# Performance work log

Hardware: AMD Instinct MI355X
Metric: run time of the kernel (lower is better)

The kernel has to match this reference:

```python
import jax, jax.numpy as jnp
import numpy as np

B, N, D, E, H = 2, 1024, 768, 128, 16
HD = D // H
INF = 1.0e6


def setup_inputs() -> dict:
    key = jax.random.key(0)
    ks = jax.random.split(key, 12)
    s = 0.02
    return {
        "node_embed": jax.random.normal(ks[0], (B, N, D), jnp.float32),
        "edge_embed": jax.random.normal(ks[1], (B, N, N, E), jnp.float32),
        "node_mask": jnp.ones((B, N), jnp.int32),
        "k_in": jax.random.normal(ks[2], (B, N, D), jnp.float32),
        "Wq": jax.random.normal(ks[3], (D, D), jnp.float32) * s,
        "bq": jnp.zeros((D,), jnp.float32),
        "Wk": jax.random.normal(ks[4], (D, D), jnp.float32) * s,
        "Wv": jax.random.normal(ks[5], (D, D), jnp.float32) * s,
        "Wg": jax.random.normal(ks[6], (D, D), jnp.float32) * s,
        "ln_g": jnp.ones((E,), jnp.float32),
        "ln_b": jnp.zeros((E,), jnp.float32),
        "Wz": jax.random.normal(ks[7], (E, H), jnp.float32) * s,
        "Wo": jax.random.normal(ks[8], (D, D), jnp.float32) * s,
    }


def reference(node_embed, edge_embed, node_mask, k_in,
              Wq, bq, Wk, Wv, Wg, ln_g, ln_b, Wz, Wo):
    b, n, d = node_embed.shape
    h = Wz.shape[1]
    hd = d // h
    # projections (torch Linear: x @ W.T + b)
    q = (node_embed @ Wq.T + bq).reshape(b, n, h, hd)
    k = (k_in @ Wk.T).reshape(b, n, h, hd)
    v = (k_in @ Wv.T).reshape(b, n, h, hd)
    g = jax.nn.sigmoid(node_embed @ Wg.T)  # (b,n,d)
    # pair bias: LayerNorm over edge_dim -> Linear(E->H) -> (b,h,i,j)
    mu = edge_embed.mean(-1, keepdims=True)
    var = edge_embed.var(-1, keepdims=True)
    zn = (edge_embed - mu) * jax.lax.rsqrt(var + 1e-5) * ln_g + ln_b
    bias = jnp.einsum('bije,eh->bhij', zn, Wz)
    # attention in fp32
    attn = jnp.einsum('bihd,bjhd->bhij', q, k) / np.sqrt(hd).astype(np.float32)
    attn = attn + bias
    attn = attn + (1.0 - node_mask[:, None, None, :].astype(jnp.float32)) * (-INF)
    attn = jax.nn.softmax(attn, axis=-1)
    o = jnp.einsum('bhij,bjhd->bihd', attn, v).reshape(b, n, d)
    return (g * o) @ Wo.T
```

## Files before the change

### kernel.cpp

```cpp
#include <hip/hip_runtime.h>
#include <hip/hip_bf16.h>

#define B_ 2
#define N_ 1024
#define D_ 768
#define E_ 128
#define H_ 16
#define HD_ 48
#define HDP_ 64

typedef short bf16x8 __attribute__((ext_vector_type(8)));
typedef float f32x4 __attribute__((ext_vector_type(4)));

__device__ __forceinline__ unsigned short f2bf(float f) {
    __hip_bfloat16 h = __float2bfloat16(f);
    return *reinterpret_cast<unsigned short*>(&h);
}
__device__ __forceinline__ float bf2f(unsigned short s) {
    return __uint_as_float(((unsigned int)s) << 16);
}

__device__ __forceinline__ void stage_tile(const float* __restrict__ edge,
                                           size_t row0, float* etbuf,
                                           int w, int lane)
{
#pragma unroll
    for (int u = 0; u < 8; ++u) {
        const int row = w * 16 + u * 2 + (lane >> 5);
        const int sl = (lane & 31) ^ (row & 7);
        const float* src = edge + (row0 + row) * E_ + (sl << 2);
        float* dst = etbuf + (w * 16 + u * 2) * E_;
        __builtin_amdgcn_global_load_lds(
            (const __attribute__((address_space(1))) void*)src,
            (__attribute__((address_space(3))) void*)dst, 16, 0, 0);
    }
}

__device__ __forceinline__ void stage64(const unsigned short* __restrict__ src,
                                        int row0, int k0,
                                        unsigned short* tile, int w, int lane)
{
#pragma unroll
    for (int u = 0; u < 2; ++u) {
        const int rloc = (lane >> 3);
        const int row = w * 16 + u * 8 + rloc;
        const int ch = (lane & 7) ^ rloc;
        const unsigned short* s = src + (size_t)(row0 + row) * D_ + k0 + ch * 8;
        unsigned short* d = tile + (w * 16 + u * 8) * 64;
        __builtin_amdgcn_global_load_lds(
            (const __attribute__((address_space(1))) void*)s,
            (__attribute__((address_space(3))) void*)d, 16, 0, 0);
    }
}

#define LDF(tile, r, gc) \
    (*(const bf16x8*)&(tile)[(size_t)(r) * 64 + ((((gc) ^ ((r) & 7))) << 3)])

__global__ __launch_bounds__(256, 2) void bias_conv_kernel(
    const float* __restrict__ edge, const float* __restrict__ lng,
    const float* __restrict__ lnb, const float* __restrict__ Wz,
    const int* __restrict__ mask, unsigned short* __restrict__ bias,
    const float* __restrict__ node, const float* __restrict__ kin,
    const float* __restrict__ Wq, const float* __restrict__ Wk,
    const float* __restrict__ Wv, const float* __restrict__ Wg,
    const float* __restrict__ Wo,
    unsigned short* __restrict__ nb, unsigned short* __restrict__ kb,
    unsigned short* __restrict__ WqB, unsigned short* __restrict__ WkB,
    unsigned short* __restrict__ WvB, unsigned short* __restrict__ WgB,
    unsigned short* __restrict__ Whi, unsigned short* __restrict__ Wlo,
    unsigned short* __restrict__ qp, unsigned short* __restrict__ kp)
{
    const int tid = threadIdx.x;
    const int lane = tid & 63;
    const int w = tid >> 6;
    const int lr = lane & 15, lg = lane >> 4;

    __shared__ __align__(16) float et[2][64 * E_];

    if (blockIdx.x >= 2048) {
        const int c = blockIdx.x - 2048;
        for (int u = c * 256 + tid; u < 1589248; u += 131072) {
            if (u < 786432) {
                const int y01 = u / 393216;
                const int idx4 = (u - y01 * 393216) * 4;
                const float* s = y01 ? kin : node;
                unsigned short* d = y01 ? kb : nb;
                const float4 v = *(const float4*)(s + idx4);
                ushort4 o;
                o.x = f2bf(v.x); o.y = f2bf(v.y); o.z = f2bf(v.z); o.w = f2bf(v.w);
                *(ushort4*)(d + idx4) = o;
            } else if (u < 1523712) {
                const int u2 = u - 786432;
                const int w5 = u2 / 147456;
                const int idx4 = (u2 - w5 * 147456) * 4;
                if (w5 < 4) {
                    const float* s = (w5 == 0) ? Wq : (w5 == 1) ? Wk :
                                     (w5 == 2) ? Wv : Wg;
                    unsigned short* d = (w5 == 0) ? WqB : (w5 == 1) ? WkB :
                                        (w5 == 2) ? WvB : WgB;
                    const float4 v = *(const float4*)(s + idx4);
                    ushort4 o;
                    o.x = f2bf(v.x); o.y = f2bf(v.y);
                    o.z = f2bf(v.z); o.w = f2bf(v.w);
                    *(ushort4*)(d + idx4) = o;
                } else {
                    const float4 v = *(const float4*)(Wo + idx4);
                    ushort4 hi, lo;
                    hi.x = f2bf(v.x); lo.x = f2bf(v.x - bf2f(hi.x));
                    hi.y = f2bf(v.y); lo.y = f2bf(v.y - bf2f(hi.y));
                    hi.z = f2bf(v.z); lo.z = f2bf(v.z - bf2f(hi.z));
                    hi.w = f2bf(v.w); lo.w = f2bf(v.w - bf2f(hi.w));
                    *(ushort4*)(Whi + idx4) = hi;
                    *(ushort4*)(Wlo + idx4) = lo;
                }
            } else {
                const int u3 = u - 1523712;
                const int row = u3 >> 1, half = u3 & 1;
                uint4 z = {0u, 0u, 0u, 0u};
                *(uint4*)(qp + ((size_t)row << 6) + 48 + half * 8) = z;
                *(uint4*)(kp + ((size_t)row << 6) + 48 + half * 8) = z;
            }
        }
        return;
    }

    bf16x8 wzf[4];
#pragma unroll
    for (int ks = 0; ks < 4; ++ks)
#pragma unroll
        for (int e = 0; e < 8; ++e)
            wzf[ks][e] = (short)f2bf(Wz[(ks * 32 + lg * 8 + e) * H_ + lr]);

    size_t t = blockIdx.x;
    stage_tile(edge, t * 64, et[0], w, lane);
    __syncthreads();

    for (int it = 0; it < 16; ++it) {
        float* cbuf = et[it & 1];
        float* nbuf = et[(it & 1) ^ 1];
        if (it < 15) stage_tile(edge, (t + 2048) * 64, nbuf, w, lane);

        const int row = w * 16 + lr;
        const int rx = row & 7;
        const float* xr = cbuf + row * E_;
        float x[4][8];
        float s = 0.f, sq = 0.f;
#pragma unroll
        for (int ks = 0; ks < 4; ++ks) {
            const int s0 = ks * 8 + lg * 2;
            const float4 a = *(const float4*)(xr + ((s0 ^ rx) << 2));
            const float4 bb = *(const float4*)(xr + (((s0 + 1) ^ rx) << 2));
            x[ks][0] = a.x; x[ks][1] = a.y; x[ks][2] = a.z; x[ks][3] = a.w;
            x[ks][4] = bb.x; x[ks][5] = bb.y; x[ks][6] = bb.z; x[ks][7] = bb.w;
#pragma unroll
            for (int e = 0; e < 8; ++e) { s += x[ks][e]; sq = fmaf(x[ks][e], x[ks][e], sq); }
        }
        s  += __shfl_xor(s, 16);  s  += __shfl_xor(s, 32);
        sq += __shfl_xor(sq, 16); sq += __shfl_xor(sq, 32);
        const float mean = s * (1.f / 128.f);
        const float var = sq * (1.f / 128.f) - mean * mean;
        const float rs = rsqrtf(var + 1e-5f);
        const float c0 = -mean * rs;

        f32x4 acc = {};
#pragma unroll
        for (int ks = 0; ks < 4; ++ks) {
            bf16x8 af;
#pragma unroll
            for (int e = 0; e < 8; ++e) {
                const int ee = ks * 32 + lg * 8 + e;
                const float zn = fmaf(fmaf(x[ks][e], rs, c0), lng[ee], lnb[ee]);
                af[e] = (short)f2bf(zn);
            }
            acc = __builtin_amdgcn_mfma_f32_16x16x32_bf16(af, wzf[ks], acc, 0, 0, 0);
        }

        const int b = (int)(t >> 14);
        const int i = (int)((t >> 4) & 1023);
        const int j = (int)((t & 15) << 6) + w * 16 + lg * 4;
        const int4 mv = *(const int4*)(mask + b * N_ + j);
        const int* mvp = (const int*)&mv;
        ushort4 pk;
        pk.x = f2bf(acc[0] + (1.f - (float)mvp[0]) * (-1.0e6f));
        pk.y = f2bf(acc[1] + (1.f - (float)mvp[1]) * (-1.0e6f));
        pk.z = f2bf(acc[2] + (1.f - (float)mvp[2]) * (-1.0e6f));
        pk.w = f2bf(acc[3] + (1.f - (float)mvp[3]) * (-1.0e6f));
        *(ushort4*)(bias + (((size_t)((b * H_ + lr) * N_ + i)) << 10) + j) = pk;

        __syncthreads();
        t += 2048;
    }
}

__global__ __launch_bounds__(256) void proj2_kernel(
    const unsigned short* __restrict__ nb, const unsigned short* __restrict__ kb,
    const unsigned short* __restrict__ WqB, const unsigned short* __restrict__ WkB,
    const unsigned short* __restrict__ WvB, const unsigned short* __restrict__ WgB,
    const float* __restrict__ bq,
    unsigned short* __restrict__ qp, unsigned short* __restrict__ kp,
    unsigned short* __restrict__ vT, float* __restrict__ g)
{
    const int pair = blockIdx.z;
    const int tid = threadIdx.x;
    const int lane = tid & 63;
    const int w = tid >> 6;
    const int wm = w >> 1, wn = w & 1;
    const int lr = lane & 15, lg = lane >> 4;
    const int mbase = blockIdx.x * 64;
    const int nbase = blockIdx.y * 64;

    const unsigned short* A  = pair ? kb  : nb;
    const unsigned short* W1 = pair ? WkB : WqB;
    const unsigned short* W2 = pair ? WvB : WgB;

    __shared__ __align__(16) unsigned short st[2][3][64 * 64];

    f32x4 acc1[2][2] = {};
    f32x4 acc2[2][2] = {};

    stage64(A,  mbase, 0, st[0][0], w, lane);
    stage64(W1, nbase, 0, st[0][1], w, lane);
    stage64(W2, nbase, 0, st[0][2], w, lane);
    __syncthreads();

    for (int ks = 0; ks < 12; ++ks) {
        unsigned short (*cb)[4096] = st[ks & 1];
        if (ks < 11) {
            unsigned short (*nbuf)[4096] = st[(ks & 1) ^ 1];
            const int k1 = (ks + 1) * 64;
            stage64(A,  mbase, k1, nbuf[0], w, lane);
            stage64(W1, nbase, k1, nbuf[1], w, lane);
            stage64(W2, nbase, k1, nbuf[2], w, lane);
        }
#pragma unroll
        for (int hf = 0; hf < 2; ++hf) {
            bf16x8 af[2], w1f[2], w2f[2];
#pragma unroll
            for (int ms = 0; ms < 2; ++ms)
                af[ms] = LDF(cb[0], wm * 32 + ms * 16 + lr, hf * 4 + lg);
#pragma unroll
            for (int ns = 0; ns < 2; ++ns) {
                w1f[ns] = LDF(cb[1], wn * 32 + ns * 16 + lr, hf * 4 + lg);
                w2f[ns] = LDF(cb[2], wn * 32 + ns * 16 + lr, hf * 4 + lg);
            }
#pragma unroll
            for (int ms = 0; ms < 2; ++ms)
#pragma unroll
                for (int ns = 0; ns < 2; ++ns) {
                    acc1[ms][ns] = __builtin_amdgcn_mfma_f32_16x16x32_bf16(
                        af[ms], w1f[ns], acc1[ms][ns], 0, 0, 0);
                    if (pair == 0)
                        acc2[ms][ns] = __builtin_amdgcn_mfma_f32_16x16x32_bf16(
                            af[ms], w2f[ns], acc2[ms][ns], 0, 0, 0);
                    else
                        acc2[ns][ms] = __builtin_amdgcn_mfma_f32_16x16x32_bf16(
                            w2f[ns], af[ms], acc2[ns][ms], 0, 0, 0);
                }
        }
        __syncthreads();
    }

    unsigned short* t1 = &st[0][0][0];
    unsigned short* t2 = &st[0][1][0];
    float* gt = (float*)&st[0][1][0];

    float bqv[2] = {0.f, 0.f};
    if (pair == 0) {
#pragma unroll
        for (int ns = 0; ns < 2; ++ns)
            bqv[ns] = bq[nbase + wn * 32 + ns * 16 + lr];
    }

#pragma unroll
    for (int ms = 0; ms < 2; ++ms)
#pragma unroll
        for (int ns = 0; ns < 2; ++ns)
#pragma unroll
            for (int r = 0; r < 4; ++r) {
                const int row = wm * 32 + ms * 16 + lg * 4 + r;
                const int col = wn * 32 + ns * 16 + lr;
                t1[row * 64 + col] = f2bf(acc1[ms][ns][r] + bqv[ns]);
                if (pair == 0)
                    gt[row * 64 + col] = 1.f / (1.f + __expf(-acc2[ms][ns][r]));
                else {
                    const int drow = wn * 32 + ns * 16 + lg * 4 + r;
                    const int tcol = wm * 32 + ms * 16 + lr;
                    t2[drow * 64 + tcol] = f2bf(acc2[ns][ms][r]);
                }
            }
    __syncthreads();

    const int b = mbase >> 10;
    const int tok0 = mbase & 1023;
    unsigned short* dst1 = (pair == 0) ? qp : kp;
    for (int c = tid; c < 512; c += 256) {
        const int row = c >> 3, ch = (c & 7) * 8;
        const int colg = nbase + ch;
        const int h = colg / HD_, hd = colg - h * HD_;
        *(uint4*)(dst1 + (((size_t)((b * H_ + h) * N_ + tok0 + row)) << 6) + hd) =
            *(const uint4*)&t1[row * 64 + ch];
    }
    if (pair == 0) {
        for (int c = tid; c < 1024; c += 256) {
            const int row = c >> 4, ch = (c & 15) * 4;
            *(float4*)(g + (size_t)(mbase + row) * D_ + nbase + ch) =
                *(const float4*)&gt[row * 64 + ch];
        }
    } else {
        for (int c = tid; c < 512; c += 256) {
            const int dl = c >> 3, tch = (c & 7) * 8;
            const int dg = nbase + dl;
            const int h = dg / HD_, hd = dg - h * HD_;
            *(uint4*)(vT + (((size_t)((b * H_ + h) * HD_ + hd)) << 10) + tok0 + tch) =
                *(const uint4*)&t2[dl * 64 + tch];
        }
    }
}

__global__ __launch_bounds__(256) void attn_kernel(
    const unsigned short* __restrict__ qp, const unsigned short* __restrict__ kp,
    const unsigned short* __restrict__ vT, const unsigned short* __restrict__ bias,
    const float* __restrict__ g,
    unsigned short* __restrict__ Xhi, unsigned short* __restrict__ Xlo)
{
    const int tid = threadIdx.x;
    const int w = tid >> 6;
    const int lane = tid & 63;
    const int lr = lane & 15, lg = lane >> 4;
    const int bh = blockIdx.x >> 6;
    const int it = blockIdx.x & 63;
    const int b = bh >> 4;
    const int h = bh & 15;
    const int i0 = it * 16;
    const float scale = 0.14433756729740643f;

    __shared__ unsigned short pt[4][16][40];
    __shared__ float comb[3][64][13];

    bf16x8 qf0, qf1;
    {
        const unsigned short* qb = qp + (((size_t)bh * N_ + i0 + lr) << 6) + lg * 8;
        qf0 = *(const bf16x8*)qb;
        qf1 = *(const bf16x8*)(qb + 32);
    }

    float li = 0.f;
    f32x4 ov[3] = {};
    const unsigned short* biasrow =
        bias + ((size_t)bh << 20) + ((size_t)(i0 + lr) << 10);

    const int jlo = w * 256;
    for (int j0 = jlo; j0 < jlo + 256; j0 += 32) {
#pragma unroll
        for (int s = 0; s < 2; ++s) {
            const unsigned short* kb =
                kp + (((size_t)bh * N_ + j0 + s * 16 + lr) << 6) + lg * 8;
            bf16x8 k0 = *(const bf16x8*)kb;
            bf16x8 k1 = *(const bf16x8*)(kb + 32);
            f32x4 tacc = {};
            tacc = __builtin_amdgcn_mfma_f32_16x16x32_bf16(k0, qf0, tacc, 0, 0, 0);
            tacc = __builtin_amdgcn_mfma_f32_16x16x32_bf16(k1, qf1, tacc, 0, 0, 0);
            const ushort4 bv = *(const ushort4*)(biasrow + j0 + s * 16 + lg * 4);
            const unsigned short* bvp = (const unsigned short*)&bv;
            float p[4];
#pragma unroll
            for (int r = 0; r < 4; ++r) {
                p[r] = __expf(fmaf(tacc[r], scale, bf2f(bvp[r])));
                li += p[r];
            }
            ushort4 pk;
            pk.x = f2bf(p[0]); pk.y = f2bf(p[1]);
            pk.z = f2bf(p[2]); pk.w = f2bf(p[3]);
            *(ushort4*)&pt[w][lr][s * 16 + lg * 4] = pk;
        }
        bf16x8 pa = *(const bf16x8*)&pt[w][lr][lg * 8];
#pragma unroll
        for (int v = 0; v < 3; ++v) {
            const unsigned short* vb =
                vT + (((size_t)(bh * HD_ + v * 16 + lr)) << 10) + j0 + lg * 8;
            bf16x8 vf = *(const bf16x8*)vb;
            ov[v] = __builtin_amdgcn_mfma_f32_16x16x32_bf16(pa, vf, ov[v], 0, 0, 0);
        }
    }

    if (w > 0) {
        float* cb = &comb[w - 1][lane][0];
#pragma unroll
        for (int v = 0; v < 3; ++v)
#pragma unroll
            for (int r = 0; r < 4; ++r) cb[v * 4 + r] = ov[v][r];
        cb[12] = li;
    }
    __syncthreads();
    if (w == 0) {
#pragma unroll
        for (int s = 0; s < 3; ++s) {
            const float* cb = &comb[s][lane][0];
#pragma unroll
            for (int v = 0; v < 3; ++v)
#pragma unroll
                for (int r = 0; r < 4; ++r) ov[v][r] += cb[v * 4 + r];
            li += cb[12];
        }
        li += __shfl_xor(li, 16);
        li += __shfl_xor(li, 32);
        float lired[4];
#pragma unroll
        for (int r = 0; r < 4; ++r) lired[r] = __shfl(li, lg * 4 + r);

#pragma unroll
        for (int v = 0; v < 3; ++v) {
#pragma unroll
            for (int r = 0; r < 4; ++r) {
                const size_t row = (size_t)(b * N_ + i0 + lg * 4 + r);
                const int col = h * HD_ + v * 16 + lr;
                const float xv = g[row * D_ + col] * (ov[v][r] / lired[r]);
                const unsigned short hi = f2bf(xv);
                const size_t off = row * D_ + col;
                Xhi[off] = hi;
                Xlo[off] = f2bf(xv - bf2f(hi));
            }
        }
    }
}

__global__ __launch_bounds__(256) void out_gemm(
    const unsigned short* __restrict__ Xhi, const unsigned short* __restrict__ Xlo,
    const unsigned short* __restrict__ Whi, const unsigned short* __restrict__ Wlo,
    float* __restrict__ out)
{
    const int tid = threadIdx.x;
    const int lane = tid & 63;
    const int w = tid >> 6;
    const int wm = w >> 1, wn = w & 1;
    const int lr = lane & 15, lg = lane >> 4;
    const int mbase = blockIdx.x * 64;
    const int nbase = blockIdx.y * 64;

    __shared__ __align__(16) unsigned short st[2][4][64 * 64];

    f32x4 acc[2][2] = {};

    stage64(Xhi, mbase, 0, st[0][0], w, lane);
    stage64(Xlo, mbase, 0, st[0][1], w, lane);
    stage64(Whi, nbase, 0, st[0][2], w, lane);
    stage64(Wlo, nbase, 0, st[0][3], w, lane);
    __syncthreads();

    for (int ks = 0; ks < 12; ++ks) {
        unsigned short (*cb)[4096] = st[ks & 1];
        if (ks < 11) {
            unsigned short (*nbuf)[4096] = st[(ks & 1) ^ 1];
            const int k1 = (ks + 1) * 64;
            stage64(Xhi, mbase, k1, nbuf[0], w, lane);
            stage64(Xlo, mbase, k1, nbuf[1], w, lane);
            stage64(Whi, nbase, k1, nbuf[2], w, lane);
            stage64(Wlo, nbase, k1, nbuf[3], w, lane);
        }
#pragma unroll
        for (int hf = 0; hf < 2; ++hf) {
            bf16x8 ah[2], al[2], bh[2], bl[2];
#pragma unroll
            for (int ms = 0; ms < 2; ++ms) {
                ah[ms] = LDF(cb[0], wm * 32 + ms * 16 + lr, hf * 4 + lg);
                al[ms] = LDF(cb[1], wm * 32 + ms * 16 + lr, hf * 4 + lg);
            }
#pragma unroll
            for (int ns = 0; ns < 2; ++ns) {
                bh[ns] = LDF(cb[2], wn * 32 + ns * 16 + lr, hf * 4 + lg);
                bl[ns] = LDF(cb[3], wn * 32 + ns * 16 + lr, hf * 4 + lg);
            }
#pragma unroll
            for (int ms = 0; ms < 2; ++ms)
#pragma unroll
                for (int ns = 0; ns < 2; ++ns) {
                    acc[ms][ns] = __builtin_amdgcn_mfma_f32_16x16x32_bf16(ah[ms], bh[ns], acc[ms][ns], 0, 0, 0);
                    acc[ms][ns] = __builtin_amdgcn_mfma_f32_16x16x32_bf16(ah[ms], bl[ns], acc[ms][ns], 0, 0, 0);
                    acc[ms][ns] = __builtin_amdgcn_mfma_f32_16x16x32_bf16(al[ms], bh[ns], acc[ms][ns], 0, 0, 0);
                }
        }
        __syncthreads();
    }

#pragma unroll
    for (int ms = 0; ms < 2; ++ms)
#pragma unroll
        for (int ns = 0; ns < 2; ++ns)
#pragma unroll
            for (int r = 0; r < 4; ++r)
                out[(size_t)(mbase + wm * 32 + ms * 16 + lg * 4 + r) * D_ +
                    nbase + wn * 32 + ns * 16 + lr] = acc[ms][ns][r];
}

extern "C" void kernel_launch(void* const* d_in, const int* in_sizes, int n_in,
                              void* d_out, int out_size, void* d_ws, size_t ws_size,
                              hipStream_t stream) {
    const float* node = (const float*)d_in[0];
    const float* edge = (const float*)d_in[1];
    const int*   mask = (const int*)d_in[2];
    const float* kin  = (const float*)d_in[3];
    const float* Wq   = (const float*)d_in[4];
    const float* bq   = (const float*)d_in[5];
    const float* Wk   = (const float*)d_in[6];
    const float* Wv   = (const float*)d_in[7];
    const float* Wg   = (const float*)d_in[8];
    const float* lng  = (const float*)d_in[9];
    const float* lnb  = (const float*)d_in[10];
    const float* Wz   = (const float*)d_in[11];
    const float* Wo   = (const float*)d_in[12];
    float* out = (float*)d_out;

    char* ws = (char*)d_ws;
    const size_t qk_bytes = (size_t)B_ * H_ * N_ * HDP_ * 2;
    unsigned short* qp = (unsigned short*)ws;   ws += qk_bytes;
    unsigned short* kp = (unsigned short*)ws;   ws += qk_bytes;
    unsigned short* vT = (unsigned short*)ws;   ws += (size_t)B_ * H_ * HD_ * N_ * 2;
    float* gbuf = (float*)ws;                   ws += (size_t)B_ * N_ * D_ * 4;
    unsigned short* bias = (unsigned short*)ws; ws += (size_t)B_ * H_ * N_ * N_ * 2;
    unsigned short* Xhi = (unsigned short*)ws;  ws += (size_t)B_ * N_ * D_ * 2;
    unsigned short* Xlo = (unsigned short*)ws;  ws += (size_t)B_ * N_ * D_ * 2;
    unsigned short* Whi = (unsigned short*)ws;  ws += (size_t)D_ * D_ * 2;
    unsigned short* Wlo = (unsigned short*)ws;  ws += (size_t)D_ * D_ * 2;
    unsigned short* nb  = (unsigned short*)ws;  ws += (size_t)B_ * N_ * D_ * 2;
    unsigned short* kb  = (unsigned short*)ws;  ws += (size_t)B_ * N_ * D_ * 2;
    unsigned short* WqB = (unsigned short*)ws;  ws += (size_t)D_ * D_ * 2;
    unsigned short* WkB = (unsigned short*)ws;  ws += (size_t)D_ * D_ * 2;
    unsigned short* WvB = (unsigned short*)ws;  ws += (size_t)D_ * D_ * 2;
    unsigned short* WgB = (unsigned short*)ws;  ws += (size_t)D_ * D_ * 2;

    bias_conv_kernel<<<dim3(2560), 256, 0, stream>>>(
        edge, lng, lnb, Wz, mask, bias,
        node, kin, Wq, Wk, Wv, Wg, Wo,
        nb, kb, WqB, WkB, WvB, WgB, Whi, Wlo, qp, kp);
    proj2_kernel<<<dim3(32, 12, 2), 256, 0, stream>>>(
        nb, kb, WqB, WkB, WvB, WgB, bq, qp, kp, vT, gbuf);
    attn_kernel<<<dim3(2048), 256, 0, stream>>>(qp, kp, vT, bias, gbuf, Xhi, Xlo);
    out_gemm<<<dim3(32, 12), 256, 0, stream>>>(Xhi, Xlo, Whi, Wlo, out);
}
```

Baseline: 329.0 us.

## Fuse QKVG projection into bias kernel with on-the-fly bf16 conversion

Merges the projection GEMM into the edge-bias kernel as extra blocks. Those blocks load fp32 node/k_in and weights directly, convert them to bf16 in registers, and stage them in shared memory. This drops the separate conversion pass, its bf16 intermediate buffers and one kernel launch, and lets the projection run alongside the bandwidth-bound bias work. In the attention kernel, the bias row loads are also hoisted ahead of the loop and the P tile is double-buffered. The costs are higher register pressure and 64KB of shared memory per block, which may reduce occupancy.

```diff
diff --git a/kernel.cpp b/kernel.cpp
--- a/kernel.cpp
+++ b/kernel.cpp
@@ -56,65 +56,187 @@
 #define LDF(tile, r, gc) \
     (*(const bf16x8*)&(tile)[(size_t)(r) * 64 + ((((gc) ^ ((r) & 7))) << 3)])
 
-__global__ __launch_bounds__(256, 2) void bias_conv_kernel(
+__global__ __launch_bounds__(256, 2) void fused_kernel(
     const float* __restrict__ edge, const float* __restrict__ lng,
     const float* __restrict__ lnb, const float* __restrict__ Wz,
     const int* __restrict__ mask, unsigned short* __restrict__ bias,
     const float* __restrict__ node, const float* __restrict__ kin,
     const float* __restrict__ Wq, const float* __restrict__ Wk,
     const float* __restrict__ Wv, const float* __restrict__ Wg,
-    const float* __restrict__ Wo,
-    unsigned short* __restrict__ nb, unsigned short* __restrict__ kb,
-    unsigned short* __restrict__ WqB, unsigned short* __restrict__ WkB,
-    unsigned short* __restrict__ WvB, unsigned short* __restrict__ WgB,
+    const float* __restrict__ Wo, const float* __restrict__ bq,
     unsigned short* __restrict__ Whi, unsigned short* __restrict__ Wlo,
-    unsigned short* __restrict__ qp, unsigned short* __restrict__ kp)
+    unsigned short* __restrict__ qp, unsigned short* __restrict__ kp,
+    unsigned short* __restrict__ vT, float* __restrict__ g)
 {
     const int tid = threadIdx.x;
     const int lane = tid & 63;
     const int w = tid >> 6;
     const int lr = lane & 15, lg = lane >> 4;
 
-    __shared__ __align__(16) float et[2][64 * E_];
-
-    if (blockIdx.x >= 2048) {
-        const int c = blockIdx.x - 2048;
-        for (int u = c * 256 + tid; u < 1589248; u += 131072) {
-            if (u < 786432) {
-                const int y01 = u / 393216;
-                const int idx4 = (u - y01 * 393216) * 4;
-                const float* s = y01 ? kin : node;
-                unsigned short* d = y01 ? kb : nb;
-                const float4 v = *(const float4*)(s + idx4);
-                ushort4 o;
-                o.x = f2bf(v.x); o.y = f2bf(v.y); o.z = f2bf(v.z); o.w = f2bf(v.w);
-                *(ushort4*)(d + idx4) = o;
-            } else if (u < 1523712) {
-                const int u2 = u - 786432;
-                const int w5 = u2 / 147456;
-                const int idx4 = (u2 - w5 * 147456) * 4;
-                if (w5 < 4) {
-                    const float* s = (w5 == 0) ? Wq : (w5 == 1) ? Wk :
-                                     (w5 == 2) ? Wv : Wg;
-                    unsigned short* d = (w5 == 0) ? WqB : (w5 == 1) ? WkB :
-                                        (w5 == 2) ? WvB : WgB;
-                    const float4 v = *(const float4*)(s + idx4);
-                    ushort4 o;
-                    o.x = f2bf(v.x); o.y = f2bf(v.y);
-                    o.z = f2bf(v.z); o.w = f2bf(v.w);
-                    *(ushort4*)(d + idx4) = o;
-                } else {
-                    const float4 v = *(const float4*)(Wo + idx4);
-                    ushort4 hi, lo;
-                    hi.x = f2bf(v.x); lo.x = f2bf(v.x - bf2f(hi.x));
-                    hi.y = f2bf(v.y); lo.y = f2bf(v.y - bf2f(hi.y));
-                    hi.z = f2bf(v.z); lo.z = f2bf(v.z - bf2f(hi.z));
-                    hi.w = f2bf(v.w); lo.w = f2bf(v.w - bf2f(hi.w));
-                    *(ushort4*)(Whi + idx4) = hi;
-                    *(ushort4*)(Wlo + idx4) = lo;
+    __shared__ __align__(16) unsigned char smem[65536];
+
+    if (blockIdx.x < 768) {
+        const int pair = blockIdx.x / 384;
+        const int rem = blockIdx.x - pair * 384;
+        const int mbase = (rem & 31) * 64;
+        const int nbase = (rem >> 5) * 64;
+        const int wm = w >> 1, wn = w & 1;
+
+        const float* A  = pair ? kin : node;
+        const float* W1 = pair ? Wk : Wq;
+        const float* W2 = pair ? Wv : Wg;
+        unsigned short* sbase = (unsigned short*)smem;
+
+        float4 ld[3][2][2];
+        auto issue = [&](int k0) {
+#pragma unroll
+            for (int t = 0; t < 3; ++t) {
+                const float* src = (t == 0) ? A : (t == 1) ? W1 : W2;
+                const int rb = (t == 0) ? mbase : nbase;
+#pragma unroll
+                for (int u = 0; u < 2; ++u) {
+                    const int uu = tid * 2 + u;
+                    const int row = uu >> 3, ch = uu & 7;
+                    const float* s = src + (size_t)(rb + row) * D_ + k0 + ch * 8;
+                    ld[t][u][0] = *(const float4*)s;
+                    ld[t][u][1] = *(const float4*)(s + 4);
                 }
+            }
+        };
+        auto commit = [&](unsigned short* base) {
+#pragma unroll
+            for (int t = 0; t < 3; ++t) {
+#pragma unroll
+                for (int u = 0; u < 2; ++u) {
+                    const int uu = tid * 2 + u;
+                    const int row = uu >> 3, ch = uu & 7;
+                    bf16x8 v;
+                    v[0] = (short)f2bf(ld[t][u][0].x);
+                    v[1] = (short)f2bf(ld[t][u][0].y);
+                    v[2] = (short)f2bf(ld[t][u][0].z);
+                    v[3] = (short)f2bf(ld[t][u][0].w);
+                    v[4] = (short)f2bf(ld[t][u][1].x);
+                    v[5] = (short)f2bf(ld[t][u][1].y);
+                    v[6] = (short)f2bf(ld[t][u][1].z);
+                    v[7] = (short)f2bf(ld[t][u][1].w);
+                    *(bf16x8*)&base[t * 4096 + row * 64 + ((ch ^ (row & 7)) << 3)] = v;
+                }
+            }
+        };
+
+        f32x4 acc1[2][2] = {};
+        f32x4 acc2[2][2] = {};
+
+        issue(0);
+        commit(sbase);
+        __syncthreads();
+
+        for (int ks = 0; ks < 12; ++ks) {
+            unsigned short* cb = sbase + (ks & 1) * 12288;
+            unsigned short* nb2 = sbase + ((ks & 1) ^ 1) * 12288;
+            if (ks < 11) issue((ks + 1) * 64);
+#pragma unroll
+            for (int hf = 0; hf < 2; ++hf) {
+                bf16x8 af[2], w1f[2], w2f[2];
+#pragma unroll
+                for (int ms = 0; ms < 2; ++ms)
+                    af[ms] = LDF(cb, wm * 32 + ms * 16 + lr, hf * 4 + lg);
+#pragma unroll
+                for (int ns = 0; ns < 2; ++ns) {
+                    w1f[ns] = LDF(cb + 4096, wn * 32 + ns * 16 + lr, hf * 4 + lg);
+                    w2f[ns] = LDF(cb + 8192, wn * 32 + ns * 16 + lr, hf * 4 + lg);
+                }
+#pragma unroll
+                for (int ms = 0; ms < 2; ++ms)
+#pragma unroll
+                    for (int ns = 0; ns < 2; ++ns) {
+                        acc1[ms][ns] = __builtin_amdgcn_mfma_f32_16x16x32_bf16(
+                            af[ms], w1f[ns], acc1[ms][ns], 0, 0, 0);
+                        if (pair == 0)
+                            acc2[ms][ns] = __builtin_amdgcn_mfma_f32_16x16x32_bf16(
+                                af[ms], w2f[ns], acc2[ms][ns], 0, 0, 0);
+                        else
+                            acc2[ns][ms] = __builtin_amdgcn_mfma_f32_16x16x32_bf16(
+                                w2f[ns], af[ms], acc2[ns][ms], 0, 0, 0);
+                    }
+            }
+            if (ks < 11) commit(nb2);
+            __syncthreads();
+        }
+
+        unsigned short* t1 = sbase;
+        unsigned short* t2 = sbase + 4096;
+        float* gt = (float*)(sbase + 4096);
+
+        float bqv[2] = {0.f, 0.f};
+        if (pair == 0) {
+#pragma unroll
+            for (int ns = 0; ns < 2; ++ns)
+                bqv[ns] = bq[nbase + wn * 32 + ns * 16 + lr];
+        }
+
+#pragma unroll
+        for (int ms = 0; ms < 2; ++ms)
+#pragma unroll
+            for (int ns = 0; ns < 2; ++ns)
+#pragma unroll
+                for (int r = 0; r < 4; ++r) {
+                    const int row = wm * 32 + ms * 16 + lg * 4 + r;
+                    const int col = wn * 32 + ns * 16 + lr;
+                    t1[row * 64 + col] = f2bf(acc1[ms][ns][r] + bqv[ns]);
+                    if (pair == 0)
+                        gt[row * 64 + col] = 1.f / (1.f + __expf(-acc2[ms][ns][r]));
+                    else {
+                        const int drow = wn * 32 + ns * 16 + lg * 4 + r;
+                        const int tcol = wm * 32 + ms * 16 + lr;
+                        t2[drow * 64 + tcol] = f2bf(acc2[ns][ms][r]);
+                    }
+                }
+        __syncthreads();
+
+        const int b = mbase >> 10;
+        const int tok0 = mbase & 1023;
+        unsigned short* dst1 = (pair == 0) ? qp : kp;
+        for (int c = tid; c < 512; c += 256) {
+            const int row = c >> 3, ch = (c & 7) * 8;
+            const int colg = nbase + ch;
+            const int h = colg / HD_, hd = colg - h * HD_;
+            *(uint4*)(dst1 + (((size_t)((b * H_ + h) * N_ + tok0 + row)) << 6) + hd) =
+                *(const uint4*)&t1[row * 64 + ch];
+        }
+        if (pair == 0) {
+            for (int c = tid; c < 1024; c += 256) {
+                const int row = c >> 4, ch = (c & 15) * 4;
+                *(float4*)(g + (size_t)(mbase + row) * D_ + nbase + ch) =
+                    *(const float4*)&gt[row * 64 + ch];
+            }
+        } else {
+            for (int c = tid; c < 512; c += 256) {
+                const int dl = c >> 3, tch = (c & 7) * 8;
+                const int dg = nbase + dl;
+                const int h = dg / HD_, hd = dg - h * HD_;
+                *(uint4*)(vT + (((size_t)((b * H_ + h) * HD_ + hd)) << 10) + tok0 + tch) =
+                    *(const uint4*)&t2[dl * 64 + tch];
+            }
+        }
+        return;
+    }
+
+    if (blockIdx.x >= 2816) {
+        const int c = blockIdx.x - 2816;
+        for (int u = c * 256 + tid; u < 212992; u += 32768) {
+            if (u < 147456) {
+                const int i4 = u * 4;
+                const float4 v = *(const float4*)(Wo + i4);
+                ushort4 hi, lo;
+                hi.x = f2bf(v.x); lo.x = f2bf(v.x - bf2f(hi.x));
+                hi.y = f2bf(v.y); lo.y = f2bf(v.y - bf2f(hi.y));
+                hi.z = f2bf(v.z); lo.z = f2bf(v.z - bf2f(hi.z));
+                hi.w = f2bf(v.w); lo.w = f2bf(v.w - bf2f(hi.w));
+                *(ushort4*)(Whi + i4) = hi;
+                *(ushort4*)(Wlo + i4) = lo;
             } else {
-                const int u3 = u - 1523712;
+                const int u3 = u - 147456;
                 const int row = u3 >> 1, half = u3 & 1;
                 uint4 z = {0u, 0u, 0u, 0u};
                 *(uint4*)(qp + ((size_t)row << 6) + 48 + half * 8) = z;
@@ -124,6 +246,9 @@
         return;
     }
 
+    float* e0 = (float*)smem;
+    float* e1 = e0 + 64 * E_;
+
     bf16x8 wzf[4];
 #pragma unroll
     for (int ks = 0; ks < 4; ++ks)
@@ -131,13 +256,13 @@
         for (int e = 0; e < 8; ++e)
             wzf[ks][e] = (short)f2bf(Wz[(ks * 32 + lg * 8 + e) * H_ + lr]);
 
-    size_t t = blockIdx.x;
-    stage_tile(edge, t * 64, et[0], w, lane);
+    size_t t = blockIdx.x - 768;
+    stage_tile(edge, t * 64, e0, w, lane);
     __syncthreads();
 
     for (int it = 0; it < 16; ++it) {
-        float* cbuf = et[it & 1];
-        float* nbuf = et[(it & 1) ^ 1];
+        float* cbuf = (it & 1) ? e1 : e0;
+        float* nbuf = (it & 1) ? e0 : e1;
         if (it < 15) stage_tile(edge, (t + 2048) * 64, nbuf, w, lane);
 
         const int row = w * 16 + lr;
@@ -189,131 +314,6 @@
 
         __syncthreads();
         t += 2048;
-    }
-}
-
-__global__ __launch_bounds__(256) void proj2_kernel(
-    const unsigned short* __restrict__ nb, const unsigned short* __restrict__ kb,
-    const unsigned short* __restrict__ WqB, const unsigned short* __restrict__ WkB,
-    const unsigned short* __restrict__ WvB, const unsigned short* __restrict__ WgB,
-    const float* __restrict__ bq,
-    unsigned short* __restrict__ qp, unsigned short* __restrict__ kp,
-    unsigned short* __restrict__ vT, float* __restrict__ g)
-{
-    const int pair = blockIdx.z;
-    const int tid = threadIdx.x;
-    const int lane = tid & 63;
-    const int w = tid >> 6;
-    const int wm = w >> 1, wn = w & 1;
-    const int lr = lane & 15, lg = lane >> 4;
-    const int mbase = blockIdx.x * 64;
-    const int nbase = blockIdx.y * 64;
-
-    const unsigned short* A  = pair ? kb  : nb;
-    const unsigned short* W1 = pair ? WkB : WqB;
-    const unsigned short* W2 = pair ? WvB : WgB;
-
-    __shared__ __align__(16) unsigned short st[2][3][64 * 64];
-
-    f32x4 acc1[2][2] = {};
-    f32x4 acc2[2][2] = {};
-
-    stage64(A,  mbase, 0, st[0][0], w, lane);
-    stage64(W1, nbase, 0, st[0][1], w, lane);
-    stage64(W2, nbase, 0, st[0][2], w, lane);
-    __syncthreads();
-
-    for (int ks = 0; ks < 12; ++ks) {
-        unsigned short (*cb)[4096] = st[ks & 1];
-        if (ks < 11) {
-            unsigned short (*nbuf)[4096] = st[(ks & 1) ^ 1];
-            const int k1 = (ks + 1) * 64;
-            stage64(A,  mbase, k1, nbuf[0], w, lane);
-            stage64(W1, nbase, k1, nbuf[1], w, lane);
-            stage64(W2, nbase, k1, nbuf[2], w, lane);
-        }
-#pragma unroll
-        for (int hf = 0; hf < 2; ++hf) {
-            bf16x8 af[2], w1f[2], w2f[2];
-#pragma unroll
-            for (int ms = 0; ms < 2; ++ms)
-                af[ms] = LDF(cb[0], wm * 32 + ms * 16 + lr, hf * 4 + lg);
-#pragma unroll
-            for (int ns = 0; ns < 2; ++ns) {
-                w1f[ns] = LDF(cb[1], wn * 32 + ns * 16 + lr, hf * 4 + lg);
-                w2f[ns] = LDF(cb[2], wn * 32 + ns * 16 + lr, hf * 4 + lg);
-            }
-#pragma unroll
-            for (int ms = 0; ms < 2; ++ms)
-#pragma unroll
-                for (int ns = 0; ns < 2; ++ns) {
-                    acc1[ms][ns] = __builtin_amdgcn_mfma_f32_16x16x32_bf16(
-                        af[ms], w1f[ns], acc1[ms][ns], 0, 0, 0);
-                    if (pair == 0)
-                        acc2[ms][ns] = __builtin_amdgcn_mfma_f32_16x16x32_bf16(
-                            af[ms], w2f[ns], acc2[ms][ns], 0, 0, 0);
-                    else
-                        acc2[ns][ms] = __builtin_amdgcn_mfma_f32_16x16x32_bf16(
-                            w2f[ns], af[ms], acc2[ns][ms], 0, 0, 0);
-                }
-        }
-        __syncthreads();
-    }
-
-    unsigned short* t1 = &st[0][0][0];
-    unsigned short* t2 = &st[0][1][0];
-    float* gt = (float*)&st[0][1][0];
-
-    float bqv[2] = {0.f, 0.f};
-    if (pair == 0) {
-#pragma unroll
-        for (int ns = 0; ns < 2; ++ns)
-            bqv[ns] = bq[nbase + wn * 32 + ns * 16 + lr];
-    }
-
-#pragma unroll
-    for (int ms = 0; ms < 2; ++ms)
-#pragma unroll
-        for (int ns = 0; ns < 2; ++ns)
-#pragma unroll
-            for (int r = 0; r < 4; ++r) {
-                const int row = wm * 32 + ms * 16 + lg * 4 + r;
-                const int col = wn * 32 + ns * 16 + lr;
-                t1[row * 64 + col] = f2bf(acc1[ms][ns][r] + bqv[ns]);
-                if (pair == 0)
-                    gt[row * 64 + col] = 1.f / (1.f + __expf(-acc2[ms][ns][r]));
-                else {
-                    const int drow = wn * 32 + ns * 16 + lg * 4 + r;
-                    const int tcol = wm * 32 + ms * 16 + lr;
-                    t2[drow * 64 + tcol] = f2bf(acc2[ns][ms][r]);
-                }
-            }
-    __syncthreads();
-
-    const int b = mbase >> 10;
-    const int tok0 = mbase & 1023;
-    unsigned short* dst1 = (pair == 0) ? qp : kp;
-    for (int c = tid; c < 512; c += 256) {
-        const int row = c >> 3, ch = (c & 7) * 8;
-        const int colg = nbase + ch;
-        const int h = colg / HD_, hd = colg - h * HD_;
-        *(uint4*)(dst1 + (((size_t)((b * H_ + h) * N_ + tok0 + row)) << 6) + hd) =
-            *(const uint4*)&t1[row * 64 + ch];
-    }
-    if (pair == 0) {
-        for (int c = tid; c < 1024; c += 256) {
-            const int row = c >> 4, ch = (c & 15) * 4;
-            *(float4*)(g + (size_t)(mbase + row) * D_ + nbase + ch) =
-                *(const float4*)&gt[row * 64 + ch];
-        }
-    } else {
-        for (int c = tid; c < 512; c += 256) {
-            const int dl = c >> 3, tch = (c & 7) * 8;
-            const int dg = nbase + dl;
-            const int h = dg / HD_, hd = dg - h * HD_;
-            *(uint4*)(vT + (((size_t)((b * H_ + h) * HD_ + hd)) << 10) + tok0 + tch) =
-                *(const uint4*)&t2[dl * 64 + tch];
-        }
     }
 }
 
@@ -334,7 +334,7 @@
     const int i0 = it * 16;
     const float scale = 0.14433756729740643f;
 
-    __shared__ unsigned short pt[4][16][40];
+    __shared__ unsigned short pt[2][4][16][40];
     __shared__ float comb[3][64][13];
 
     bf16x8 qf0, qf1;
@@ -344,13 +344,23 @@
         qf1 = *(const bf16x8*)(qb + 32);
     }
 
+    const unsigned short* biasrow =
+        bias + ((size_t)bh << 20) + ((size_t)(i0 + lr) << 10);
+    const int jlo = w * 256;
+
+    ushort4 bvv[8][2];
+#pragma unroll
+    for (int t8 = 0; t8 < 8; ++t8)
+#pragma unroll
+        for (int s = 0; s < 2; ++s)
+            bvv[t8][s] = *(const ushort4*)(biasrow + jlo + t8 * 32 + s * 16 + lg * 4);
+
     float li = 0.f;
     f32x4 ov[3] = {};
-    const unsigned short* biasrow =
-        bias + ((size_t)bh << 20) + ((size_t)(i0 + lr) << 10);
-
-    const int jlo = w * 256;
-    for (int j0 = jlo; j0 < jlo + 256; j0 += 32) {
+
+#pragma unroll
+    for (int t8 = 0; t8 < 8; ++t8) {
+        const int j0 = jlo + t8 * 32;
 #pragma unroll
         for (int s = 0; s < 2; ++s) {
             const unsigned short* kb =
@@ -360,8 +370,7 @@
             f32x4 tacc = {};
             tacc = __builtin_amdgcn_mfma_f32_16x16x32_bf16(k0, qf0, tacc, 0, 0, 0);
             tacc = __builtin_amdgcn_mfma_f32_16x16x32_bf16(k1, qf1, tacc, 0, 0, 0);
-            const ushort4 bv = *(const ushort4*)(biasrow + j0 + s * 16 + lg * 4);
-            const unsigned short* bvp = (const unsigned short*)&bv;
+            const unsigned short* bvp = (const unsigned short*)&bvv[t8][s];
             float p[4];
 #pragma unroll
             for (int r = 0; r < 4; ++r) {
@@ -371,9 +380,9 @@
             ushort4 pk;
             pk.x = f2bf(p[0]); pk.y = f2bf(p[1]);
             pk.z = f2bf(p[2]); pk.w = f2bf(p[3]);
-            *(ushort4*)&pt[w][lr][s * 16 + lg * 4] = pk;
-        }
-        bf16x8 pa = *(const bf16x8*)&pt[w][lr][lg * 8];
+            *(ushort4*)&pt[t8 & 1][w][lr][s * 16 + lg * 4] = pk;
+        }
+        bf16x8 pa = *(const bf16x8*)&pt[t8 & 1][w][lr][lg * 8];
 #pragma unroll
         for (int v = 0; v < 3; ++v) {
             const unsigned short* vb =
@@ -521,19 +530,11 @@
     unsigned short* Xlo = (unsigned short*)ws;  ws += (size_t)B_ * N_ * D_ * 2;
     unsigned short* Whi = (unsigned short*)ws;  ws += (size_t)D_ * D_ * 2;
     unsigned short* Wlo = (unsigned short*)ws;  ws += (size_t)D_ * D_ * 2;
-    unsigned short* nb  = (unsigned short*)ws;  ws += (size_t)B_ * N_ * D_ * 2;
-    unsigned short* kb  = (unsigned short*)ws;  ws += (size_t)B_ * N_ * D_ * 2;
-    unsigned short* WqB = (unsigned short*)ws;  ws += (size_t)D_ * D_ * 2;
-    unsigned short* WkB = (unsigned short*)ws;  ws += (size_t)D_ * D_ * 2;
-    unsigned short* WvB = (unsigned short*)ws;  ws += (size_t)D_ * D_ * 2;
-    unsigned short* WgB = (unsigned short*)ws;  ws += (size_t)D_ * D_ * 2;
-
-    bias_conv_kernel<<<dim3(2560), 256, 0, stream>>>(
+
+    fused_kernel<<<dim3(2944), 256, 0, stream>>>(
         edge, lng, lnb, Wz, mask, bias,
-        node, kin, Wq, Wk, Wv, Wg, Wo,
-        nb, kb, WqB, WkB, WvB, WgB, Whi, Wlo, qp, kp);
-    proj2_kernel<<<dim3(32, 12, 2), 256, 0, stream>>>(
-        nb, kb, WqB, WkB, WvB, WgB, bq, qp, kp, vT, gbuf);
+        node, kin, Wq, Wk, Wv, Wg, Wo, bq,
+        Whi, Wlo, qp, kp, vT, gbuf);
     attn_kernel<<<dim3(2048), 256, 0, stream>>>(qp, kp, vT, bias, gbuf, Xhi, Xlo);
     out_gemm<<<dim3(32, 12), 256, 0, stream>>>(Xhi, Xlo, Whi, Wlo, out);
 }
```

After: 346.3 us. 1.05x slower.
